# Kernel optimization log

Measured on AMD Instinct MI355X. Metric: run time of the kernel, lower is better.

The kernel has to match this reference:

```python
import jax, jax.numpy as jnp
import numpy as np

SIGMA = 2.0
INF = 1.0e6


def setup_inputs() -> dict:
    key = jax.random.key(0)
    ks = jax.random.split(key, 6)
    M, N, H, C_IN, C_OUT, K = 50000, 50000, 32, 128, 128, 15
    q_pts = jax.random.normal(ks[0], (M, 3), dtype=jnp.float32)
    s_pts = jax.random.normal(ks[1], (N, 3), dtype=jnp.float32)
    s_feats = jax.random.normal(ks[2], (N, C_IN), dtype=jnp.float32)
    neighb_inds = jax.random.randint(ks[3], (M, H), 0, N)
    weights = jax.random.normal(ks[4], (K, C_IN, C_OUT), dtype=jnp.float32) * 0.05
    kernel_points = jax.random.normal(ks[5], (K, 3), dtype=jnp.float32)
    return {"q_pts": q_pts, "s_pts": s_pts, "s_feats": s_feats,
            "neighb_inds": neighb_inds, "weights": weights,
            "kernel_points": kernel_points}


def reference(q_pts, s_pts, s_feats, neighb_inds, weights, kernel_points):
    # Pad support points with a far-away shadow point and features with zeros
    s_pts_pad = jnp.concatenate([s_pts, jnp.full((1, s_pts.shape[1]), INF, s_pts.dtype)], axis=0)
    feats_pad = jnp.concatenate([s_feats, jnp.zeros((1, s_feats.shape[1]), s_feats.dtype)], axis=0)

    # Gather neighbors: (M, H, 3) relative positions, (M, H, C) features
    neighbors = s_pts_pad[neighb_inds] - q_pts[:, None, :]
    neighbor_feats = feats_pad[neighb_inds]

    # Kernel point influences (linear): (M, H, K)
    sq_dists = jnp.sum((neighbors[:, :, None, :] - kernel_points[None, None, :, :]) ** 2, axis=-1)
    influence = jnp.clip(1.0 - jnp.sqrt(sq_dists) / SIGMA, 0.0, None)

    # Aggregate neighbor features per kernel point: (M, K, C_in)
    weighted_feats = jnp.einsum('mhk,mhc->mkc', influence, neighbor_feats)

    # Per-kernel-point matmul summed over K (groups=1): (M, C_out)
    out = jnp.einsum('mkc,kcd->md', weighted_feats, weights)
    return out
```

## Files before the change

kernel.cpp:

```cpp
#include <hip/hip_runtime.h>
#include <cmath>


constexpr int HN = 32;
constexpr int KP = 15;
constexpr int CI = 128;
constexpr int CO = 128;
constexpr int MB = 32;
constexpr int NT = 1024;
constexpr float INV_SIGMA = 0.5f;

using short8 = __attribute__((ext_vector_type(8))) short;
using f32x4  = __attribute__((ext_vector_type(4))) float;

static __device__ __forceinline__ unsigned short f2bf(float x) {
    unsigned u = __float_as_uint(x);
    u += 0x7fff + ((u >> 16) & 1);
    return (unsigned short)(u >> 16);
}
static __device__ __forceinline__ float bf2f(unsigned short h) {
    return __uint_as_float(((unsigned)h) << 16);
}

__global__ void kpconv_prep_w(const float* __restrict__ w,
                              unsigned short* __restrict__ ws16) {
    int t = blockIdx.x * blockDim.x + threadIdx.x;
    int fb = t >> 6, lane = t & 63;
    if (fb >= 480) return;
    int k = fb >> 5, s = (fb >> 3) & 3, dt = fb & 7;
    int g = lane >> 4, n = lane & 15;
    unsigned short* base = ws16 + fb * 1024 + lane * 8;
    #pragma unroll
    for (int j = 0; j < 8; ++j) {
        int c = s * 32 + g * 8 + j;
        int d = dt * 16 + n;
        float v = w[(k * CI + c) * CO + d];
        unsigned short hi = f2bf(v);
        unsigned short lo = f2bf(v - bf2f(hi));
        base[j]       = (short)hi;
        base[512 + j] = (short)lo;
    }
}

#define MFMA(a, b, c) c = __builtin_amdgcn_mfma_f32_16x16x32_bf16(a, b, c, 0, 0, 0)

__global__ __launch_bounds__(NT, 4)
void kpconv_main(const float* __restrict__ q_pts,
                 const float* __restrict__ s_pts,
                 const float* __restrict__ s_feats,
                 const int*   __restrict__ nb,
                 const float* __restrict__ kpts,
                 const unsigned short* __restrict__ wfr,
                 float* __restrict__ out, int M)
{
    __shared__ __align__(16) char pool[65536];
    float* infl = (float*)pool;

    const int t  = threadIdx.x;
    const int m0 = blockIdx.x * MB;

    {
        int p = t >> 5, h = t & 31;
        int r = m0 + p;
        bool valid = (r < M);
        int rr = valid ? r : 0;
        int idx = nb[rr * HN + h];
        float sx = s_pts[idx * 3 + 0], sy = s_pts[idx * 3 + 1], sz = s_pts[idx * 3 + 2];
        float qx = q_pts[rr * 3 + 0],  qy = q_pts[rr * 3 + 1],  qz = q_pts[rr * 3 + 2];
        float rx = sx - qx, ry = sy - qy, rz = sz - qz;
        float vals[16];
        #pragma unroll
        for (int k = 0; k < KP; ++k) {
            float dx = rx - kpts[k * 3 + 0];
            float dy = ry - kpts[k * 3 + 1];
            float dz = rz - kpts[k * 3 + 2];
            float d2 = dx * dx + dy * dy + dz * dz;
            float v  = fmaxf(1.0f - sqrtf(d2) * INV_SIGMA, 0.0f);
            vals[k] = valid ? v : 0.0f;
        }
        vals[15] = 0.0f;
        float4* dst = (float4*)(infl + (p * 32 + h) * 16);
        dst[0] = make_float4(vals[0],  vals[1],  vals[2],  vals[3]);
        dst[1] = make_float4(vals[4],  vals[5],  vals[6],  vals[7]);
        dst[2] = make_float4(vals[8],  vals[9],  vals[10], vals[11]);
        dst[3] = make_float4(vals[12], vals[13], vals[14], vals[15]);
    }
    __syncthreads();

    const int p  = t >> 5;
    const int cq = t & 31;
    float wf[KP][4];
    #pragma unroll
    for (int k = 0; k < KP; ++k) { wf[k][0]=0.f; wf[k][1]=0.f; wf[k][2]=0.f; wf[k][3]=0.f; }

    {
        int r = m0 + p;
        int rr = (r < M) ? r : 0;
        const int* nbrow = nb + rr * HN;
        const float4* f4 = (const float4*)s_feats;
        #pragma unroll 2
        for (int h = 0; h < HN; ++h) {
            int idx = nbrow[h];
            float4 f = f4[idx * (CI / 4) + cq];
            const float4* iv = (const float4*)(infl + (p * 32 + h) * 16);
            float4 a0 = iv[0], a1 = iv[1], a2 = iv[2], a3 = iv[3];
#define FMA4(kk, s)                               \
            wf[kk][0] = fmaf((s), f.x, wf[kk][0]); \
            wf[kk][1] = fmaf((s), f.y, wf[kk][1]); \
            wf[kk][2] = fmaf((s), f.z, wf[kk][2]); \
            wf[kk][3] = fmaf((s), f.w, wf[kk][3]);
            FMA4(0,  a0.x) FMA4(1,  a0.y) FMA4(2,  a0.z) FMA4(3,  a0.w)
            FMA4(4,  a1.x) FMA4(5,  a1.y) FMA4(6,  a1.z) FMA4(7,  a1.w)
            FMA4(8,  a2.x) FMA4(9,  a2.y) FMA4(10, a2.z) FMA4(11, a2.w)
            FMA4(12, a3.x) FMA4(13, a3.y) FMA4(14, a3.z)
#undef FMA4
        }
    }

    const int lane = t & 63;
    const int wid  = t >> 6;
    const int dh   = wid & 3;
    const int kq   = wid >> 2;
    const int g    = lane >> 4;
    const int n16  = lane & 15;

    f32x4 acc[2][2] = {};

    #pragma unroll
    for (int kb = 0; kb < 4; ++kb) {
        __syncthreads();
        #pragma unroll
        for (int kk = 0; kk < 4; ++kk) {
            int k = kb * 4 + kk;
            if (k < KP) {
                unsigned short h0 = f2bf(wf[k][0]), h1 = f2bf(wf[k][1]);
                unsigned short h2 = f2bf(wf[k][2]), h3 = f2bf(wf[k][3]);
                unsigned short l0 = f2bf(wf[k][0] - bf2f(h0));
                unsigned short l1 = f2bf(wf[k][1] - bf2f(h1));
                unsigned short l2 = f2bf(wf[k][2] - bf2f(h2));
                unsigned short l3 = f2bf(wf[k][3] - bf2f(h3));
                int lin = p * 256 + cq * 8;
                lin ^= (p & 7) << 4;
                uint2 hv, lv;
                hv.x = (unsigned)h0 | ((unsigned)h1 << 16);
                hv.y = (unsigned)h2 | ((unsigned)h3 << 16);
                lv.x = (unsigned)l0 | ((unsigned)l1 << 16);
                lv.y = (unsigned)l2 | ((unsigned)l3 << 16);
                *(uint2*)(pool + kk * 16384 +        lin) = hv;
                *(uint2*)(pool + kk * 16384 + 8192 + lin) = lv;
            }
        }
        __syncthreads();
        int k = kb * 4 + kq;
        if (k < KP) {
            #pragma unroll
            for (int s = 0; s < 4; ++s) {
                short8 ah[2], al[2];
                #pragma unroll
                for (int mt = 0; mt < 2; ++mt) {
                    int row = mt * 16 + n16;
                    int lin = row * 256 + s * 64 + g * 16;
                    lin ^= (row & 7) << 4;
                    ah[mt] = *(const short8*)(pool + kq * 16384 +        lin);
                    al[mt] = *(const short8*)(pool + kq * 16384 + 8192 + lin);
                }
                const unsigned short* fb0 = wfr + (((k * 4 + s) * 8 + dh * 2) * 1024) + lane * 8;
                short8 bh0 = *(const short8*)(fb0);
                short8 bl0 = *(const short8*)(fb0 + 512);
                short8 bh1 = *(const short8*)(fb0 + 1024);
                short8 bl1 = *(const short8*)(fb0 + 1536);
                MFMA(ah[0], bh0, acc[0][0]);
                MFMA(ah[0], bl0, acc[0][0]);
                MFMA(al[0], bh0, acc[0][0]);
                MFMA(ah[0], bh1, acc[0][1]);
                MFMA(ah[0], bl1, acc[0][1]);
                MFMA(al[0], bh1, acc[0][1]);
                MFMA(ah[1], bh0, acc[1][0]);
                MFMA(ah[1], bl0, acc[1][0]);
                MFMA(al[1], bh0, acc[1][0]);
                MFMA(ah[1], bh1, acc[1][1]);
                MFMA(ah[1], bl1, acc[1][1]);
                MFMA(al[1], bh1, acc[1][1]);
            }
        }
    }

    __syncthreads();
    float* red = (float*)pool;
    #pragma unroll
    for (int mt = 0; mt < 2; ++mt) {
        #pragma unroll
        for (int dti = 0; dti < 2; ++dti) {
            #pragma unroll
            for (int q = 0; q < 4; ++q) {
                int row = mt * 16 + g * 4 + q;
                int col = (dh * 2 + dti) * 16 + n16;
                red[(kq * 32 + row) * 128 + col] = acc[mt][dti][q];
            }
        }
    }
    __syncthreads();
    {
        int op = t >> 5, od = t & 31;
        const float4* r4 = (const float4*)red;
        float4 s0 = r4[(0 * 32 + op) * 32 + od];
        float4 s1 = r4[(1 * 32 + op) * 32 + od];
        float4 s2 = r4[(2 * 32 + op) * 32 + od];
        float4 s3 = r4[(3 * 32 + op) * 32 + od];
        float4 rv;
        rv.x = s0.x + s1.x + s2.x + s3.x;
        rv.y = s0.y + s1.y + s2.y + s3.y;
        rv.z = s0.z + s1.z + s2.z + s3.z;
        rv.w = s0.w + s1.w + s2.w + s3.w;
        if (m0 + op < M)
            ((float4*)out)[(m0 + op) * (CO / 4) + od] = rv;
    }
}

extern "C" void kernel_launch(void* const* d_in, const int* in_sizes, int n_in,
                              void* d_out, int out_size, void* d_ws, size_t ws_size,
                              hipStream_t stream)
{
    const float* q_pts   = (const float*)d_in[0];
    const float* s_pts   = (const float*)d_in[1];
    const float* s_feats = (const float*)d_in[2];
    const int*   nb      = (const int*)d_in[3];
    const float* weights = (const float*)d_in[4];
    const float* kpts    = (const float*)d_in[5];
    float*       out     = (float*)d_out;
    unsigned short* wpak = (unsigned short*)d_ws;

    int M = in_sizes[0] / 3;

    hipLaunchKernelGGL(kpconv_prep_w, dim3(120), dim3(256), 0, stream, weights, wpak);

    int grid = (M + MB - 1) / MB;
    hipLaunchKernelGGL(kpconv_main, dim3(grid), dim3(NT), 0, stream,
                       q_pts, s_pts, s_feats, nb, kpts, wpak, out, M);
}
```

Before: 323.0 us.

## Compute neighbor-feature aggregation with split-bf16 MFMA instead of scalar FMAs

```diff
diff --git a/kernel.cpp b/kernel.cpp
--- a/kernel.cpp
+++ b/kernel.cpp
@@ -44,7 +44,7 @@
 
 #define MFMA(a, b, c) c = __builtin_amdgcn_mfma_f32_16x16x32_bf16(a, b, c, 0, 0, 0)
 
-__global__ __launch_bounds__(NT, 4)
+__global__ __launch_bounds__(NT)
 void kpconv_main(const float* __restrict__ q_pts,
                  const float* __restrict__ s_pts,
                  const float* __restrict__ s_feats,
@@ -54,133 +54,122 @@
                  float* __restrict__ out, int M)
 {
     __shared__ __align__(16) char pool[65536];
-    float* infl = (float*)pool;
-
-    const int t  = threadIdx.x;
-    const int m0 = blockIdx.x * MB;
-
-    {
-        int p = t >> 5, h = t & 31;
-        int r = m0 + p;
-        bool valid = (r < M);
-        int rr = valid ? r : 0;
-        int idx = nb[rr * HN + h];
-        float sx = s_pts[idx * 3 + 0], sy = s_pts[idx * 3 + 1], sz = s_pts[idx * 3 + 2];
-        float qx = q_pts[rr * 3 + 0],  qy = q_pts[rr * 3 + 1],  qz = q_pts[rr * 3 + 2];
-        float rx = sx - qx, ry = sy - qy, rz = sz - qz;
-        float vals[16];
-        #pragma unroll
-        for (int k = 0; k < KP; ++k) {
-            float dx = rx - kpts[k * 3 + 0];
-            float dy = ry - kpts[k * 3 + 1];
-            float dz = rz - kpts[k * 3 + 2];
+
+    const int t    = threadIdx.x;
+    const int lane = t & 63;
+    const int wid  = t >> 6;
+    const int g    = lane >> 4;
+    const int kk   = lane & 15;
+    const int m0   = blockIdx.x * MB;
+
+    const float kx = kpts[kk * 3 + 0];
+    const float ky = kpts[kk * 3 + 1];
+    const float kz = kpts[kk * 3 + 2];
+
+    f32x4 accA[2][8] = {};
+
+    #pragma unroll
+    for (int pi = 0; pi < 2; ++pi) {
+        const int  gp    = m0 + wid * 2 + pi;
+        const bool valid = (gp < M);
+        const int  rr    = valid ? gp : 0;
+        const float qx = q_pts[rr * 3 + 0];
+        const float qy = q_pts[rr * 3 + 1];
+        const float qz = q_pts[rr * 3 + 2];
+
+        int idx[8];
+        #pragma unroll
+        for (int j = 0; j < 8; ++j) idx[j] = nb[rr * HN + g * 8 + j];
+
+        short8 Ih, Il;
+        #pragma unroll
+        for (int j = 0; j < 8; ++j) {
+            const float* sp = s_pts + idx[j] * 3;
+            float rx = sp[0] - qx, ry = sp[1] - qy, rz = sp[2] - qz;
+            float dx = rx - kx, dy = ry - ky, dz = rz - kz;
             float d2 = dx * dx + dy * dy + dz * dz;
             float v  = fmaxf(1.0f - sqrtf(d2) * INV_SIGMA, 0.0f);
-            vals[k] = valid ? v : 0.0f;
-        }
-        vals[15] = 0.0f;
-        float4* dst = (float4*)(infl + (p * 32 + h) * 16);
-        dst[0] = make_float4(vals[0],  vals[1],  vals[2],  vals[3]);
-        dst[1] = make_float4(vals[4],  vals[5],  vals[6],  vals[7]);
-        dst[2] = make_float4(vals[8],  vals[9],  vals[10], vals[11]);
-        dst[3] = make_float4(vals[12], vals[13], vals[14], vals[15]);
-    }
-    __syncthreads();
-
-    const int p  = t >> 5;
-    const int cq = t & 31;
-    float wf[KP][4];
-    #pragma unroll
-    for (int k = 0; k < KP; ++k) { wf[k][0]=0.f; wf[k][1]=0.f; wf[k][2]=0.f; wf[k][3]=0.f; }
-
-    {
-        int r = m0 + p;
-        int rr = (r < M) ? r : 0;
-        const int* nbrow = nb + rr * HN;
-        const float4* f4 = (const float4*)s_feats;
-        #pragma unroll 2
-        for (int h = 0; h < HN; ++h) {
-            int idx = nbrow[h];
-            float4 f = f4[idx * (CI / 4) + cq];
-            const float4* iv = (const float4*)(infl + (p * 32 + h) * 16);
-            float4 a0 = iv[0], a1 = iv[1], a2 = iv[2], a3 = iv[3];
-#define FMA4(kk, s)                               \
-            wf[kk][0] = fmaf((s), f.x, wf[kk][0]); \
-            wf[kk][1] = fmaf((s), f.y, wf[kk][1]); \
-            wf[kk][2] = fmaf((s), f.z, wf[kk][2]); \
-            wf[kk][3] = fmaf((s), f.w, wf[kk][3]);
-            FMA4(0,  a0.x) FMA4(1,  a0.y) FMA4(2,  a0.z) FMA4(3,  a0.w)
-            FMA4(4,  a1.x) FMA4(5,  a1.y) FMA4(6,  a1.z) FMA4(7,  a1.w)
-            FMA4(8,  a2.x) FMA4(9,  a2.y) FMA4(10, a2.z) FMA4(11, a2.w)
-            FMA4(12, a3.x) FMA4(13, a3.y) FMA4(14, a3.z)
-#undef FMA4
-        }
-    }
-
-    const int lane = t & 63;
-    const int wid  = t >> 6;
-    const int dh   = wid & 3;
-    const int kq   = wid >> 2;
-    const int g    = lane >> 4;
-    const int n16  = lane & 15;
-
-    f32x4 acc[2][2] = {};
-
-    #pragma unroll
-    for (int kb = 0; kb < 4; ++kb) {
+            if (kk == 15 || !valid) v = 0.0f;
+            unsigned short hi = f2bf(v);
+            Ih[j] = (short)hi;
+            Il[j] = (short)f2bf(v - bf2f(hi));
+        }
+
+        #pragma unroll
+        for (int ct = 0; ct < 8; ++ct) {
+            float f[8];
+            #pragma unroll
+            for (int j = 0; j < 8; ++j)
+                f[j] = s_feats[idx[j] * CI + ct * 16 + kk];
+            short8 Fh, Fl;
+            #pragma unroll
+            for (int j = 0; j < 8; ++j) {
+                unsigned short hi = f2bf(f[j]);
+                Fh[j] = (short)hi;
+                Fl[j] = (short)f2bf(f[j] - bf2f(hi));
+            }
+            MFMA(Ih, Fh, accA[pi][ct]);
+            MFMA(Ih, Fl, accA[pi][ct]);
+            MFMA(Il, Fh, accA[pi][ct]);
+        }
+    }
+
+    const int kq = wid >> 2;
+    const int dh = wid & 3;
+    f32x4 accB[2][2] = {};
+
+    #pragma unroll
+    for (int tr = 0; tr < 4; ++tr) {
+        if (tr) __syncthreads();
+        #pragma unroll
+        for (int pi = 0; pi < 2; ++pi) {
+            const int prow = wid * 2 + pi;
+            char* rowbase = pool + g * 16384 + prow * 256;
+            const int rowx = (prow & 7) << 4;
+            #pragma unroll
+            for (int ct = 0; ct < 8; ++ct) {
+                float v = accA[pi][ct][tr];
+                unsigned short hi = f2bf(v);
+                unsigned short lo = f2bf(v - bf2f(hi));
+                int c2  = (ct * 16 + kk) * 2;
+                int off = (c2 ^ (g << 5)) ^ rowx;
+                *(unsigned short*)(rowbase + off)        = hi;
+                *(unsigned short*)(rowbase + 8192 + off) = lo;
+            }
+        }
         __syncthreads();
-        #pragma unroll
-        for (int kk = 0; kk < 4; ++kk) {
-            int k = kb * 4 + kk;
-            if (k < KP) {
-                unsigned short h0 = f2bf(wf[k][0]), h1 = f2bf(wf[k][1]);
-                unsigned short h2 = f2bf(wf[k][2]), h3 = f2bf(wf[k][3]);
-                unsigned short l0 = f2bf(wf[k][0] - bf2f(h0));
-                unsigned short l1 = f2bf(wf[k][1] - bf2f(h1));
-                unsigned short l2 = f2bf(wf[k][2] - bf2f(h2));
-                unsigned short l3 = f2bf(wf[k][3] - bf2f(h3));
-                int lin = p * 256 + cq * 8;
-                lin ^= (p & 7) << 4;
-                uint2 hv, lv;
-                hv.x = (unsigned)h0 | ((unsigned)h1 << 16);
-                hv.y = (unsigned)h2 | ((unsigned)h3 << 16);
-                lv.x = (unsigned)l0 | ((unsigned)l1 << 16);
-                lv.y = (unsigned)l2 | ((unsigned)l3 << 16);
-                *(uint2*)(pool + kk * 16384 +        lin) = hv;
-                *(uint2*)(pool + kk * 16384 + 8192 + lin) = lv;
-            }
-        }
-        __syncthreads();
-        int k = kb * 4 + kq;
+        const int k = 4 * kq + tr;
         if (k < KP) {
             #pragma unroll
-            for (int s = 0; s < 4; ++s) {
+            for (int sc = 0; sc < 4; ++sc) {
                 short8 ah[2], al[2];
                 #pragma unroll
                 for (int mt = 0; mt < 2; ++mt) {
-                    int row = mt * 16 + n16;
-                    int lin = row * 256 + s * 64 + g * 16;
-                    lin ^= (row & 7) << 4;
-                    ah[mt] = *(const short8*)(pool + kq * 16384 +        lin);
-                    al[mt] = *(const short8*)(pool + kq * 16384 + 8192 + lin);
+                    int row = mt * 16 + kk;
+                    int c2  = sc * 64 + g * 16;
+                    int off = (c2 ^ (kq << 5)) ^ ((row & 7) << 4);
+                    const char* base = pool + kq * 16384 + row * 256 + off;
+                    ah[mt] = *(const short8*)(base);
+                    al[mt] = *(const short8*)(base + 8192);
                 }
-                const unsigned short* fb0 = wfr + (((k * 4 + s) * 8 + dh * 2) * 1024) + lane * 8;
+                const unsigned short* fb0 =
+                    wfr + ((k * 4 + sc) * 8 + dh * 2) * 1024 + lane * 8;
                 short8 bh0 = *(const short8*)(fb0);
                 short8 bl0 = *(const short8*)(fb0 + 512);
                 short8 bh1 = *(const short8*)(fb0 + 1024);
                 short8 bl1 = *(const short8*)(fb0 + 1536);
-                MFMA(ah[0], bh0, acc[0][0]);
-                MFMA(ah[0], bl0, acc[0][0]);
-                MFMA(al[0], bh0, acc[0][0]);
-                MFMA(ah[0], bh1, acc[0][1]);
-                MFMA(ah[0], bl1, acc[0][1]);
-                MFMA(al[0], bh1, acc[0][1]);
-                MFMA(ah[1], bh0, acc[1][0]);
-                MFMA(ah[1], bl0, acc[1][0]);
-                MFMA(al[1], bh0, acc[1][0]);
-                MFMA(ah[1], bh1, acc[1][1]);
-                MFMA(ah[1], bl1, acc[1][1]);
-                MFMA(al[1], bh1, acc[1][1]);
+                MFMA(ah[0], bh0, accB[0][0]);
+                MFMA(ah[0], bl0, accB[0][0]);
+                MFMA(al[0], bh0, accB[0][0]);
+                MFMA(ah[0], bh1, accB[0][1]);
+                MFMA(ah[0], bl1, accB[0][1]);
+                MFMA(al[0], bh1, accB[0][1]);
+                MFMA(ah[1], bh0, accB[1][0]);
+                MFMA(ah[1], bl0, accB[1][0]);
+                MFMA(al[1], bh0, accB[1][0]);
+                MFMA(ah[1], bh1, accB[1][1]);
+                MFMA(ah[1], bl1, accB[1][1]);
+                MFMA(al[1], bh1, accB[1][1]);
             }
         }
     }
@@ -194,8 +183,8 @@
             #pragma unroll
             for (int q = 0; q < 4; ++q) {
                 int row = mt * 16 + g * 4 + q;
-                int col = (dh * 2 + dti) * 16 + n16;
-                red[(kq * 32 + row) * 128 + col] = acc[mt][dti][q];
+                int col = (dh * 2 + dti) * 16 + kk;
+                red[(kq * 32 + row) * 128 + col] = accB[mt][dti][q];
             }
         }
     }
```

Result: faster. 305.5 us (-5.4%).
